# Optimization experiments

Measured on AMD Instinct MI355X. Metric: run time of the kernel, lower is better.

## Reference

```python
import jax, jax.numpy as jnp
import numpy as np

B, N, K = 8, 1024, 20


def _w(key, o, i):
    return jax.random.normal(key, (o, i), dtype=jnp.float32) * (1.0 / np.sqrt(i))


def setup_inputs() -> dict:
    key = jax.random.key(0)
    ks = iter(jax.random.split(key, 64))
    d = {"inputs": jax.random.normal(next(ks), (B, 3, N, 1), dtype=jnp.float32)}
    shapes = {
        "he_w1": (32, 12), "he_w2": (64, 32), "hn_w1": (32, 67), "hn_w2": (64, 32),
        "b1e_w1": (48, 192), "b1e_w2": (128, 48), "b1n_w1": (48, 192), "b1n_w2": (128, 48),
        "b2e_w1": (96, 384), "b2e_w2": (192, 96), "b2n_w1": (96, 320), "b2n_w2": (192, 96),
        "f_w": (512, 384), "p1_w": (256, 512), "p2_w": (128, 256), "p3_w": (40, 128),
    }
    for name, (o, i) in shapes.items():
        d[name] = _w(next(ks), o, i)
        d[name.replace("_w", "_b")] = jnp.zeros((o,), dtype=jnp.float32)
    return d


def _conv(x, w, b):
    # BasicConv with norm=None: 1x1 Conv2d + bias. x: [B,C,N,k]
    return jnp.einsum('bcnk,oc->bonk', x, w) + b[None, :, None, None]


def _conv_relu(x, w, b):
    return jax.nn.relu(_conv(x, w, b))


def _gather(x, idx):
    # batched_index_select: x [B,C,N,1], idx [B,N,k] -> [B,C,N,k]
    b, c, n, _ = x.shape
    k = idx.shape[-1]
    out = jnp.take_along_axis(x[:, :, :, 0], idx.reshape(b, 1, n * k), axis=2)
    return out.reshape(b, c, n, k)


def _knn(x, k):
    # DenseKnnGraph: x [B,C,N,1] -> (nn_idx, center_idx), each [B,N,k]
    xt = jnp.transpose(x[:, :, :, 0], (0, 2, 1))  # [B,N,C]
    sq = jnp.sum(xt * xt, axis=-1, keepdims=True)
    dist = sq - 2.0 * jnp.einsum('bnc,bmc->bnm', xt, xt) + jnp.transpose(sq, (0, 2, 1))
    _, nn_idx = jax.lax.top_k(-dist, k)
    center = jnp.broadcast_to(jnp.arange(x.shape[2])[None, :, None], nn_idx.shape)
    return nn_idx, center


def _mp(nf, e_ij, nn_idx, center, ew1, eb1, ew2, eb2, nw1, nb1, nw2, nb2):
    # MessagePassing block (Kearnes et al. style)
    h_i = _gather(nf, center)  # [B,Cin,N,k]
    h_j = _gather(nf, nn_idx)
    e_p = _conv_relu(_conv_relu(jnp.concatenate([e_ij, h_i, h_j], axis=1), ew1, eb1), ew2, eb2)
    m = jnp.broadcast_to(jnp.sum(e_p, axis=3, keepdims=True),
                         e_p.shape[:3] + (h_i.shape[-1],))
    h_p = _conv_relu(_conv_relu(jnp.concatenate([h_i, m], axis=1), nw1, nb1), nw2, nb2)
    return h_p[:, :, :, 0:1], e_p


def reference(inputs, he_w1, he_b1, he_w2, he_b2, hn_w1, hn_b1, hn_w2, hn_b2,
              b1e_w1, b1e_b1, b1e_w2, b1e_b2, b1n_w1, b1n_b1, b1n_w2, b1n_b2,
              b2e_w1, b2e_b1, b2e_w2, b2e_b2, b2n_w1, b2n_b1, b2n_w2, b2n_b2,
              f_w, f_b, p1_w, p1_b, p2_w, p2_b, p3_w, p3_b):
    nn_idx, center = _knn(inputs[:, 0:3], K)
    # initial edge features: (h_i, h_i - h_j) on xyz-KNN graph
    gh_i = _gather(inputs, center)
    gh_j = _gather(inputs, nn_idx)
    e_ij = jnp.concatenate([gh_i, gh_i - gh_j], axis=1)  # [B, 2*in, N, k]
    h1, e1 = _mp(inputs, e_ij, nn_idx, center, he_w1, he_b1, he_w2, he_b2, hn_w1, hn_b1, hn_w2, hn_b2)
    h2, e2 = _mp(h1, e1, nn_idx, center, b1e_w1, b1e_b1, b1e_w2, b1e_b2, b1n_w1, b1n_b1, b1n_w2, b1n_b2)
    h3, e3 = _mp(h2, e2, nn_idx, center, b2e_w1, b2e_b1, b2e_w2, b2e_b2, b2n_w1, b2n_b1, b2n_w2, b2n_b2)
    feats = jnp.concatenate([h1, h2, h3], axis=1)  # [B, 384, N, 1]
    fus = _conv_relu(feats, f_w, f_b)  # [B, 512, N, 1]
    pooled = jnp.max(fus, axis=(2, 3), keepdims=True)  # max_pool2d over [N,1]
    # prediction head (dropout = identity at inference)
    pred = _conv(_conv_relu(_conv_relu(pooled, p1_w, p1_b), p2_w, p2_b), p3_w, p3_b)
    return pred[:, :, :, 0], inputs  # (logits [B,n_classes,1], edge_features)
```

## Files before the change

kernel.cpp:

```cpp
#include <hip/hip_runtime.h>

#define BDIM 8
#define NDIM 1024
#define KNN 20

typedef unsigned short u16;
typedef float f32x4 __attribute__((ext_vector_type(4)));
typedef short short8 __attribute__((ext_vector_type(8)));
typedef unsigned short ushort8 __attribute__((ext_vector_type(8)));

__device__ inline u16 f2bf(float f) {
  unsigned u = __float_as_uint(f);
  unsigned r = (u + 0x7fffu + ((u >> 16) & 1u)) >> 16;
  return (u16)r;
}
__device__ inline float bf2f(u16 v) {
  return __uint_as_float(((unsigned)v) << 16);
}

__global__ __launch_bounds__(512) void knn_wcvt(
    const float* __restrict__ x, int* __restrict__ nn,
    const float* __restrict__ w1_3, const float* __restrict__ w2_3,
    const float* __restrict__ w1_2, const float* __restrict__ w2_2,
    const float* __restrict__ hn_w1, const float* __restrict__ f_w,
    const float* __restrict__ he_w1, const float* __restrict__ he_w2,
    const float* __restrict__ bn_w1, const float* __restrict__ bn_w2,
    const float* __restrict__ n2_w1, const float* __restrict__ n2_w2,
    u16* __restrict__ w1b3e, u16* __restrict__ wpq3, u16* __restrict__ w2b3,
    u16* __restrict__ w1b2e, u16* __restrict__ wpq2, u16* __restrict__ w2b2,
    float* __restrict__ w1p1, u16* __restrict__ fwb,
    u16* __restrict__ w1b1, u16* __restrict__ w2b1,
    u16* __restrict__ wn1b, u16* __restrict__ wn2b,
    u16* __restrict__ wn21b, u16* __restrict__ wn22b,
    int* __restrict__ pooled) {
  const int tid = threadIdx.x;
  if (blockIdx.x >= BDIM * 128) {
    const int idx = (blockIdx.x - BDIM * 128) * 512 + tid;
    if (idx < 512 * 384) fwb[idx] = f2bf(f_w[idx]);
    if (idx < 96 * 128) {
      int oc = idx >> 7, c = idx & 127;
      w1b3e[idx] = f2bf(w1_3[oc * 384 + c]);
    }
    if (idx < 192 * 128) {
      int n = idx >> 7, c = idx & 127;
      wpq3[idx] = f2bf(n < 96 ? w1_3[n * 384 + 128 + c]
                              : w1_3[(n - 96) * 384 + 256 + c]);
    }
    if (idx < 192 * 96) w2b3[idx] = f2bf(w2_3[idx]);
    if (idx < 48 * 64) {
      int oc = idx >> 6, c = idx & 63;
      w1b2e[idx] = f2bf(w1_2[oc * 192 + c]);
    }
    if (idx < 96 * 64) {
      int n = idx >> 6, c = idx & 63;
      wpq2[idx] = f2bf(n < 48 ? w1_2[n * 192 + 64 + c]
                              : w1_2[(n - 48) * 192 + 128 + c]);
    }
    if (idx < 128 * 64) {
      int oc = idx >> 6, i = idx & 63;
      w2b2[idx] = (i < 48) ? f2bf(w2_2[oc * 48 + i]) : (u16)0;
    }
    if (idx < 32 * 68) {
      int oc = idx / 68, c = idx - oc * 68;
      w1p1[idx] = (c < 67) ? hn_w1[oc * 67 + c] : 0.0f;
    }
    if (idx < 32 * 32) {
      int oc = idx >> 5, c = idx & 31;
      w1b1[idx] = (c < 12) ? f2bf(he_w1[oc * 12 + c]) : (u16)0;
    }
    if (idx < 64 * 32) w2b1[idx] = f2bf(he_w2[idx]);
    if (idx < 96 * 320) wn1b[idx] = f2bf(bn_w1[idx]);
    if (idx < 192 * 96) wn2b[idx] = f2bf(bn_w2[idx]);
    if (idx < 48 * 192) wn21b[idx] = f2bf(n2_w1[idx]);
    if (idx < 128 * 64) {
      int oc = idx >> 6, i = idx & 63;
      wn22b[idx] = (i < 48) ? f2bf(n2_w2[oc * 48 + i]) : (u16)0;
    }
    if (idx < BDIM * 512) pooled[idx] = 0;
    return;
  }
  {
#pragma clang fp contract(off)
    __shared__ float xs0[NDIM], xs1[NDIM], xs2[NDIM], sq[NDIM];
    const int lane = tid & 63;
    const int w = tid >> 6;
    const int b = blockIdx.x >> 7;
    const int n = ((blockIdx.x & 127) << 3) + w;
    for (int i = tid; i < NDIM; i += 512) {
      float a0 = x[(b * 3 + 0) * NDIM + i];
      float a1 = x[(b * 3 + 1) * NDIM + i];
      float a2 = x[(b * 3 + 2) * NDIM + i];
      xs0[i] = a0; xs1[i] = a1; xs2[i] = a2;
      sq[i] = (a0 * a0 + a1 * a1) + a2 * a2;
    }
    __syncthreads();
    const float xn0 = xs0[n], xn1 = xs1[n], xn2 = xs2[n], sqn = sq[n];
    float dl[16];
#pragma unroll
    for (int t = 0; t < 16; ++t) {
      int m = t * 64 + lane;
      float dot = (xn0 * xs0[m] + xn1 * xs1[m]) + xn2 * xs2[m];
      dl[t] = (sqn - 2.0f * dot) + sq[m];
    }
    int* nnrow = &nn[(b * NDIM + n) * KNN];
    for (int r = 0; r < KNN; ++r) {
      float bd = dl[0];
      int bt = 0;
#pragma unroll
      for (int t = 1; t < 16; ++t) {
        if (dl[t] < bd) { bd = dl[t]; bt = t; }
      }
      int bi = bt * 64 + lane;
#pragma unroll
      for (int off = 1; off < 64; off <<= 1) {
        float pd = __shfl_xor(bd, off);
        int pi = __shfl_xor(bi, off);
        if (pd < bd || (pd == bd && pi < bi)) { bd = pd; bi = pi; }
      }
      if (lane == 0) nnrow[r] = bi;
      if ((bi & 63) == lane) {
        int wt = bi >> 6;
#pragma unroll
        for (int t = 0; t < 16; ++t) {
          if (t == wt) dl[t] = 3.4e38f;
        }
      }
    }
  }
}

template <int PTS, int CE, int CMID, int COUT, bool WRITE_E, bool FIRST>
__global__ __launch_bounds__(256) void edge_mfma(
    const u16* __restrict__ eprev, const float* __restrict__ finput,
    const int* __restrict__ nnb, const u16* __restrict__ w1b,
    const float* __restrict__ b1v, const u16* __restrict__ w2b,
    const float* __restrict__ b2v, const u16* __restrict__ pq,
    u16* __restrict__ eout, float* __restrict__ mout) {
  constexpr int K2 = (CMID + 31) & ~31;
  constexpr int NPQ = 2 * CMID;
  constexpr int MT = PTS * KNN;
  constexpr int MTL = MT / 16;
  constexpr int XPB = CE + 8;
  constexpr int QYP = K2 + 8;
  __shared__ u16 Xs[MT * XPB];
  __shared__ u16 QY[MT * QYP];
  __shared__ float pld[FIRST ? 8 : PTS * CMID];
  const int tid = threadIdx.x;
  const int lane = tid & 63;
  const int wv = tid >> 6;
  const int q = lane >> 4;
  const int bn0 = blockIdx.x * PTS;
  const int b = bn0 >> 10;
  if constexpr (FIRST) {
    for (int idx = tid; idx < MT * (CE / 8); idx += 256) {
      int p = idx / (CE / 8), kc = idx - p * (CE / 8);
      int k0 = kc * 8;
      int bn = bn0 + p / KNN;
      int n = bn & (NDIM - 1);
      int j = nnb[(size_t)bn0 * KNN + p];
      ushort8 r;
#pragma unroll
      for (int t = 0; t < 8; ++t) {
        int c = k0 + t;
        float v = 0.0f;
        if (c < 3) v = finput[(b * 3 + c) * NDIM + n];
        else if (c < 6)
          v = finput[(b * 3 + c - 3) * NDIM + n] -
              finput[(b * 3 + c - 3) * NDIM + j];
        else if (c < 9) v = finput[(b * 3 + c - 6) * NDIM + n];
        else if (c < 12) v = finput[(b * 3 + c - 9) * NDIM + j];
        r[t] = f2bf(v);
      }
      *(ushort8*)&Xs[p * XPB + k0] = r;
    }
  } else {
    constexpr int KC = CE / 8;
    for (int ch = tid; ch < MT * KC; ch += 256) {
      int p = ch / KC, kc = ch - p * KC;
      int k0 = kc * 8;
      *(uint4*)&Xs[p * XPB + k0] =
          *(const uint4*)&eprev[((size_t)blockIdx.x * MT + p) * CE + k0];
    }
    constexpr int QC = CMID / 8;
    for (int i = tid; i < MT * QC; i += 256) {
      int p = i / QC, c8 = (i - p * QC) * 8;
      int j = nnb[(size_t)bn0 * KNN + p];
      *(uint4*)&QY[p * QYP + c8] =
          *(const uint4*)&pq[((size_t)(b << 10) + j) * NPQ + CMID + c8];
    }
    if constexpr (K2 != CMID) {
      constexpr int PC = (K2 - CMID) / 8;
      for (int i = tid; i < MT * PC; i += 256) {
        int p = i / PC, c8 = CMID + (i - p * PC) * 8;
        uint4 z = {0, 0, 0, 0};
        *(uint4*)&QY[p * QYP + c8] = z;
      }
    }
    for (int i = tid; i < PTS * CMID; i += 256) {
      int pt = i / CMID, c = i - pt * CMID;
      pld[i] = bf2f(pq[(size_t)(bn0 + pt) * NPQ + c]) + b1v[c];
    }
  }
  __syncthreads();
  {
    constexpr int NT1 = CMID / 16;
    constexpr int J1 = MTL * NT1;
    constexpr int KS1 = CE / 32;
    for (int job = wv; job < J1; job += 4) {
      int mt = job / NT1, nt = job - mt * NT1;
      int row = mt * 16 + (lane & 15);
      int ncol = nt * 16 + (lane & 15);
      int kb = q * 8;
      f32x4 acc = {0.f, 0.f, 0.f, 0.f};
      const u16* ap = &Xs[row * XPB + kb];
      const u16* bp = &w1b[(size_t)ncol * CE + kb];
#pragma unroll
      for (int ks = 0; ks < KS1; ++ks) {
        short8 a = *(const short8*)(ap + ks * 32);
        short8 bb = *(const short8*)(bp + ks * 32);
        acc = __builtin_amdgcn_mfma_f32_16x16x32_bf16(a, bb, acc, 0, 0, 0);
      }
      int m0 = mt * 16 + q * 4;
      if constexpr (FIRST) {
        float bias = b1v[ncol];
#pragma unroll
        for (int r = 0; r < 4; ++r) {
          float yv = fmaxf(acc[r] + bias, 0.0f);
          QY[(m0 + r) * QYP + ncol] = f2bf(yv);
        }
      } else {
        int pt = m0 / KNN;
        float padd = pld[pt * CMID + ncol];
#pragma unroll
        for (int r = 0; r < 4; ++r) {
          int m = m0 + r;
          float qadd = bf2f(QY[m * QYP + ncol]);
          float yv = fmaxf(acc[r] + padd + qadd, 0.0f);
          QY[m * QYP + ncol] = f2bf(yv);
        }
      }
    }
  }
  __syncthreads();
  {
    constexpr int NT2 = COUT / 16;
    constexpr int KS2 = K2 / 32;
    for (int nt = wv; nt < NT2; nt += 4) {
      int ncol = nt * 16 + (lane & 15);
      int kb = q * 8;
      short8 bfrag[KS2];
      const u16* bp = &w2b[(size_t)ncol * K2 + kb];
#pragma unroll
      for (int ks = 0; ks < KS2; ++ks)
        bfrag[ks] = *(const short8*)(bp + ks * 32);
      float bias = b2v[ncol];
      float s[PTS];
#pragma unroll
      for (int pt = 0; pt < PTS; ++pt) s[pt] = 0.0f;
#pragma unroll
      for (int mt = 0; mt < MTL; ++mt) {
        f32x4 acc = {0.f, 0.f, 0.f, 0.f};
        const u16* ap = &QY[(mt * 16 + (lane & 15)) * QYP + kb];
#pragma unroll
        for (int ks = 0; ks < KS2; ++ks) {
          short8 a = *(const short8*)(ap + ks * 32);
          acc = __builtin_amdgcn_mfma_f32_16x16x32_bf16(a, bfrag[ks], acc, 0, 0, 0);
        }
        int m0 = mt * 16 + q * 4;
        float part = 0.0f;
#pragma unroll
        for (int r = 0; r < 4; ++r) {
          float yv = fmaxf(acc[r] + bias, 0.0f);
          if (WRITE_E)
            eout[((size_t)blockIdx.x * MT + m0 + r) * COUT + ncol] = f2bf(yv);
          part += yv;
        }
        int ptA = (4 * mt) / 5;
        int ptB = (4 * mt + 3) / 5;
        int qb = 5 * ptB - 4 * mt;
#pragma unroll
        for (int pt2 = 0; pt2 < PTS; ++pt2) {
          if (pt2 == ptA && ptA == ptB) s[pt2] += part;
          else if (pt2 == ptA) s[pt2] += (q < qb) ? part : 0.0f;
          else if (pt2 == ptB) s[pt2] += (q < qb) ? 0.0f : part;
        }
      }
#pragma unroll
      for (int pt = 0; pt < PTS; ++pt) {
        float sv = s[pt];
        sv += __shfl_xor(sv, 16);
        sv += __shfl_xor(sv, 32);
        if (lane < 16)
          mout[(size_t)(bn0 + pt) * COUT + nt * 16 + lane] = sv;
      }
    }
  }
}

template <int TP, int CH, int CM, int CINP, int CMID, int COUT, int NPQ, bool FIRSTH>
__global__ __launch_bounds__(256) void node_conv(
    const float* __restrict__ h, const float* __restrict__ inputs,
    const float* __restrict__ mbuf, const float* __restrict__ w1p,
    const float* __restrict__ b1v, const float* __restrict__ w2,
    const float* __restrict__ b2v, float* __restrict__ hout,
    const u16* __restrict__ wpq, u16* __restrict__ pq) {
  constexpr int CIN = CH + CM;
  constexpr int XP = CINP + 4;
  constexpr int Y1P = CMID + 4;
  constexpr int PG = TP / 4;
  constexpr int HP = COUT + 8;
  __shared__ float Xs[TP * XP];
  __shared__ float Y1s[TP * Y1P];
  __shared__ u16 Hb[(NPQ > 0) ? TP * HP : 8];
  const int tid = threadIdx.x;
  const int bn0 = blockIdx.x * TP;
  if constexpr (FIRSTH) {
    for (int idx = tid; idx < TP * CIN; idx += 256) {
      int p = idx / CIN, c = idx - p * CIN;
      int bn = bn0 + p;
      int b = bn >> 10, n = bn & (NDIM - 1);
      Xs[p * XP + c] = (c < CH) ? inputs[(b * 3 + c) * NDIM + n]
                                : mbuf[(size_t)bn * CM + (c - CH)];
    }
    if constexpr (CINP > CIN) {
      constexpr int PAD = CINP - CIN;
      for (int idx = tid; idx < TP * PAD; idx += 256) {
        int p = idx / PAD, c = CIN + idx % PAD;
        Xs[p * XP + c] = 0.0f;
      }
    }
  } else {
    constexpr int C4 = CIN / 4;
    for (int idx = tid; idx < TP * C4; idx += 256) {
      int p = idx / C4, c = (idx - p * C4) * 4;
      int bn = bn0 + p;
      float4 v = (c < CH) ? *(const float4*)&h[(size_t)bn * CH + c]
                          : *(const float4*)&mbuf[(size_t)bn * CM + (c - CH)];
      *(float4*)&Xs[p * XP + c] = v;
    }
  }
  __syncthreads();
  {
    constexpr int NT1 = PG * (CMID / 4);
    for (int t = tid; t < NT1; t += 256) {
      int pg = t % PG, og = t / PG;
      float acc[4][4];
#pragma unroll
      for (int j = 0; j < 4; ++j) {
        float bj = b1v[og * 4 + j];
#pragma unroll
        for (int i = 0; i < 4; ++i) acc[i][j] = bj;
      }
      for (int cin = 0; cin < CINP; cin += 4) {
        float4 xr[4], wr[4];
#pragma unroll
        for (int i = 0; i < 4; ++i)
          xr[i] = *(const float4*)&Xs[(pg * 4 + i) * XP + cin];
#pragma unroll
        for (int j = 0; j < 4; ++j)
          wr[j] = *(const float4*)&w1p[(size_t)(og * 4 + j) * CINP + cin];
#pragma unroll
        for (int i = 0; i < 4; ++i)
#pragma unroll
          for (int j = 0; j < 4; ++j) {
            acc[i][j] += xr[i].x * wr[j].x;
            acc[i][j] += xr[i].y * wr[j].y;
            acc[i][j] += xr[i].z * wr[j].z;
            acc[i][j] += xr[i].w * wr[j].w;
          }
      }
#pragma unroll
      for (int i = 0; i < 4; ++i)
#pragma unroll
        for (int j = 0; j < 4; ++j)
          Y1s[(pg * 4 + i) * Y1P + og * 4 + j] = fmaxf(acc[i][j], 0.0f);
    }
  }
  __syncthreads();
  {
    constexpr int NT2 = PG * (COUT / 4);
    for (int t = tid; t < NT2; t += 256) {
      int pg = t % PG, og = t / PG;
      float acc[4][4];
#pragma unroll
      for (int j = 0; j < 4; ++j) {
        float bj = b2v[og * 4 + j];
#pragma unroll
        for (int i = 0; i < 4; ++i) acc[i][j] = bj;
      }
      for (int cin = 0; cin < CMID; cin += 4) {
        float4 xr[4], wr[4];
#pragma unroll
        for (int i = 0; i < 4; ++i)
          xr[i] = *(const float4*)&Y1s[(pg * 4 + i) * Y1P + cin];
#pragma unroll
        for (int j = 0; j < 4; ++j)
          wr[j] = *(const float4*)&w2[(size_t)(og * 4 + j) * CMID + cin];
#pragma unroll
        for (int i = 0; i < 4; ++i)
#pragma unroll
          for (int j = 0; j < 4; ++j) {
            acc[i][j] += xr[i].x * wr[j].x;
            acc[i][j] += xr[i].y * wr[j].y;
            acc[i][j] += xr[i].z * wr[j].z;
            acc[i][j] += xr[i].w * wr[j].w;
          }
      }
#pragma unroll
      for (int i = 0; i < 4; ++i) {
        int bn = bn0 + pg * 4 + i;
#pragma unroll
        for (int j = 0; j < 4; ++j) {
          float v = fmaxf(acc[i][j], 0.0f);
          hout[(size_t)bn * COUT + og * 4 + j] = v;
          if constexpr (NPQ > 0) Hb[(pg * 4 + i) * HP + og * 4 + j] = f2bf(v);
        }
      }
    }
  }
  if constexpr (NPQ > 0) {
    __syncthreads();
    const int lane = tid & 63;
    const int wv = tid >> 6;
    constexpr int NT = NPQ / 16;
    constexpr int JOBS = (TP / 16) * NT;
    constexpr int KS = COUT / 32;
    for (int job = wv; job < JOBS; job += 4) {
      int mt = job / NT, nt = job - mt * NT;
      int row = mt * 16 + (lane & 15);
      int ncol = nt * 16 + (lane & 15);
      int kb = (lane >> 4) * 8;
      f32x4 acc = {0.f, 0.f, 0.f, 0.f};
      const u16* ap = &Hb[row * HP + kb];
      const u16* bp = &wpq[(size_t)ncol * COUT + kb];
#pragma unroll
      for (int ks = 0; ks < KS; ++ks) {
        short8 a = *(const short8*)(ap + ks * 32);
        short8 bb = *(const short8*)(bp + ks * 32);
        acc = __builtin_amdgcn_mfma_f32_16x16x32_bf16(a, bb, acc, 0, 0, 0);
      }
      int m0 = mt * 16 + (lane >> 4) * 4;
#pragma unroll
      for (int r = 0; r < 4; ++r)
        pq[(size_t)(bn0 + m0 + r) * NPQ + ncol] = f2bf(acc[r]);
    }
  }
}

__global__ __launch_bounds__(256) void node2_mfma(
    const float* __restrict__ h1, const float* __restrict__ m2,
    const u16* __restrict__ w1b, const float* __restrict__ b1v,
    const u16* __restrict__ w2b, const float* __restrict__ b2v,
    float* __restrict__ h2out, const u16* __restrict__ wpq,
    u16* __restrict__ pq) {
  constexpr int TP = 32, XP = 200, Y1P = 72, HP = 136;
  __shared__ u16 Xb[TP * XP];
  __shared__ u16 Y1[TP * Y1P];
  __shared__ u16 Hb[TP * HP];
  const int tid = threadIdx.x;
  const int lane = tid & 63;
  const int wv = tid >> 6;
  const int q = lane >> 4;
  const int bn0 = blockIdx.x * TP;
  for (int i = tid; i < TP * 24; i += 256) {
    int p = i / 24, kc = i - p * 24;
    int k0 = kc * 8;
    const float* src = (k0 < 64) ? &h1[(size_t)(bn0 + p) * 64 + k0]
                                 : &m2[(size_t)(bn0 + p) * 128 + (k0 - 64)];
    float4 f0 = *(const float4*)src;
    float4 f1 = *(const float4*)(src + 4);
    ushort8 r;
    r[0] = f2bf(f0.x); r[1] = f2bf(f0.y); r[2] = f2bf(f0.z); r[3] = f2bf(f0.w);
    r[4] = f2bf(f1.x); r[5] = f2bf(f1.y); r[6] = f2bf(f1.z); r[7] = f2bf(f1.w);
    *(ushort8*)&Xb[p * XP + k0] = r;
  }
  for (int i = tid; i < TP * 2; i += 256) {
    int p = i >> 1, c8 = 48 + (i & 1) * 8;
    ushort8 z = {0, 0, 0, 0, 0, 0, 0, 0};
    *(ushort8*)&Y1[p * Y1P + c8] = z;
  }
  __syncthreads();
  for (int job = wv; job < 6; job += 4) {
    int mt = job / 3, nt = job - mt * 3;
    int row = mt * 16 + (lane & 15);
    int ncol = nt * 16 + (lane & 15);
    int kb = q * 8;
    f32x4 acc = {0.f, 0.f, 0.f, 0.f};
    const u16* ap = &Xb[row * XP + kb];
    const u16* bp = &w1b[(size_t)ncol * 192 + kb];
#pragma unroll
    for (int ks = 0; ks < 6; ++ks) {
      short8 a = *(const short8*)(ap + ks * 32);
      short8 bb = *(const short8*)(bp + ks * 32);
      acc = __builtin_amdgcn_mfma_f32_16x16x32_bf16(a, bb, acc, 0, 0, 0);
    }
    float bias = b1v[ncol];
    int m0 = mt * 16 + q * 4;
#pragma unroll
    for (int r = 0; r < 4; ++r)
      Y1[(m0 + r) * Y1P + ncol] = f2bf(fmaxf(acc[r] + bias, 0.0f));
  }
  __syncthreads();
  for (int job = wv; job < 16; job += 4) {
    int mt = job / 8, nt = job - mt * 8;
    int row = mt * 16 + (lane & 15);
    int ncol = nt * 16 + (lane & 15);
    int kb = q * 8;
    f32x4 acc = {0.f, 0.f, 0.f, 0.f};
    const u16* ap = &Y1[row * Y1P + kb];
    const u16* bp = &w2b[(size_t)ncol * 64 + kb];
#pragma unroll
    for (int ks = 0; ks < 2; ++ks) {
      short8 a = *(const short8*)(ap + ks * 32);
      short8 bb = *(const short8*)(bp + ks * 32);
      acc = __builtin_amdgcn_mfma_f32_16x16x32_bf16(a, bb, acc, 0, 0, 0);
    }
    float bias = b2v[ncol];
    int m0 = mt * 16 + q * 4;
#pragma unroll
    for (int r = 0; r < 4; ++r) {
      float v = fmaxf(acc[r] + bias, 0.0f);
      h2out[(size_t)(bn0 + m0 + r) * 128 + ncol] = v;
      Hb[(m0 + r) * HP + ncol] = f2bf(v);
    }
  }
  __syncthreads();
  for (int job = wv; job < 24; job += 4) {
    int mt = job / 12, nt = job - mt * 12;
    int row = mt * 16 + (lane & 15);
    int ncol = nt * 16 + (lane & 15);
    int kb = q * 8;
    f32x4 acc = {0.f, 0.f, 0.f, 0.f};
    const u16* ap = &Hb[row * HP + kb];
    const u16* bp = &wpq[(size_t)ncol * 128 + kb];
#pragma unroll
    for (int ks = 0; ks < 4; ++ks) {
      short8 a = *(const short8*)(ap + ks * 32);
      short8 bb = *(const short8*)(bp + ks * 32);
      acc = __builtin_amdgcn_mfma_f32_16x16x32_bf16(a, bb, acc, 0, 0, 0);
    }
    int m0 = mt * 16 + q * 4;
#pragma unroll
    for (int r = 0; r < 4; ++r)
      pq[(size_t)(bn0 + m0 + r) * 192 + ncol] = f2bf(acc[r]);
  }
}

__global__ __launch_bounds__(256) void fuse_pool_mfma(
    const float* __restrict__ h1, const float* __restrict__ h2,
    const float* __restrict__ m3, const u16* __restrict__ wn1b,
    const float* __restrict__ bn1v, const u16* __restrict__ wn2b,
    const float* __restrict__ bn2v, const u16* __restrict__ fwb,
    const float* __restrict__ fb, int* __restrict__ pooled) {
  constexpr int TP = 32;
  constexpr int XNP = 328;
  constexpr int Y1NP = 104;
  constexpr int XPB = 392;
  __shared__ __align__(16) char smem[TP * XPB * 2];
  u16* Xs = (u16*)smem;
  u16* Xn = (u16*)smem;
  __shared__ u16 Y1n[TP * Y1NP];
  __shared__ int pmax[512];
  const int tid = threadIdx.x;
  const int lane = tid & 63;
  const int wv = tid >> 6;
  const int q = lane >> 4;
  const int bn0 = blockIdx.x * TP;
  const int b = bn0 >> 10;
  for (int i = tid; i < 512; i += 256) pmax[i] = 0;
  for (int i = tid; i < TP * 41; i += 256) {
    int p = i / 41, kc = i - p * 41;
    int k0 = kc * 8;
    ushort8 r;
    if (kc < 16) {
      const float* src = &h2[(size_t)(bn0 + p) * 128 + k0];
      float4 f0 = *(const float4*)src;
      float4 f1 = *(const float4*)(src + 4);
      r[0] = f2bf(f0.x); r[1] = f2bf(f0.y); r[2] = f2bf(f0.z); r[3] = f2bf(f0.w);
      r[4] = f2bf(f1.x); r[5] = f2bf(f1.y); r[6] = f2bf(f1.z); r[7] = f2bf(f1.w);
    } else if (kc < 40) {
      const float* src = &m3[(size_t)(bn0 + p) * 192 + (k0 - 128)];
      float4 f0 = *(const float4*)src;
      float4 f1 = *(const float4*)(src + 4);
      r[0] = f2bf(f0.x); r[1] = f2bf(f0.y); r[2] = f2bf(f0.z); r[3] = f2bf(f0.w);
      r[4] = f2bf(f1.x); r[5] = f2bf(f1.y); r[6] = f2bf(f1.z); r[7] = f2bf(f1.w);
    } else {
#pragma unroll
      for (int t = 0; t < 8; ++t) r[t] = 0;
    }
    *(ushort8*)&Xn[p * XNP + k0] = r;
  }
  __syncthreads();
  for (int job = wv; job < 12; job += 4) {
    int mt = job / 6, nt = job - mt * 6;
    int row = mt * 16 + (lane & 15);
    int ncol = nt * 16 + (lane & 15);
    int kb = q * 8;
    f32x4 acc = {0.f, 0.f, 0.f, 0.f};
    const u16* ap = &Xn[row * XNP + kb];
    const u16* bp = &wn1b[(size_t)ncol * 320 + kb];
#pragma unroll
    for (int ks = 0; ks < 10; ++ks) {
      short8 a = *(const short8*)(ap + ks * 32);
      short8 bb = *(const short8*)(bp + ks * 32);
      acc = __builtin_amdgcn_mfma_f32_16x16x32_bf16(a, bb, acc, 0, 0, 0);
    }
    float bias = bn1v[ncol];
    int m0 = mt * 16 + q * 4;
#pragma unroll
    for (int r = 0; r < 4; ++r)
      Y1n[(m0 + r) * Y1NP + ncol] = f2bf(fmaxf(acc[r] + bias, 0.0f));
  }
  __syncthreads();
  for (int i = tid; i < TP * 24; i += 256) {
    int p = i / 24, kc = i - p * 24;
    int k0 = kc * 8;
    const float* src = (k0 < 64) ? &h1[(size_t)(bn0 + p) * 64 + k0]
                                 : &h2[(size_t)(bn0 + p) * 128 + (k0 - 64)];
    float4 f0 = *(const float4*)src;
    float4 f1 = *(const float4*)(src + 4);
    ushort8 r;
    r[0] = f2bf(f0.x); r[1] = f2bf(f0.y); r[2] = f2bf(f0.z); r[3] = f2bf(f0.w);
    r[4] = f2bf(f1.x); r[5] = f2bf(f1.y); r[6] = f2bf(f1.z); r[7] = f2bf(f1.w);
    *(ushort8*)&Xs[p * XPB + k0] = r;
  }
  if (tid < TP) {
    ushort8 z = {0, 0, 0, 0, 0, 0, 0, 0};
    *(ushort8*)&Xs[tid * XPB + 384] = z;
  }
  for (int job = wv; job < 24; job += 4) {
    int mt = job / 12, nt = job - mt * 12;
    int row = mt * 16 + (lane & 15);
    int ncol = nt * 16 + (lane & 15);
    int kb = q * 8;
    f32x4 acc = {0.f, 0.f, 0.f, 0.f};
    const u16* ap = &Y1n[row * Y1NP + kb];
    const u16* bp = &wn2b[(size_t)ncol * 96 + kb];
#pragma unroll
    for (int ks = 0; ks < 3; ++ks) {
      short8 a = *(const short8*)(ap + ks * 32);
      short8 bb = *(const short8*)(bp + ks * 32);
      acc = __builtin_amdgcn_mfma_f32_16x16x32_bf16(a, bb, acc, 0, 0, 0);
    }
    float bias = bn2v[ncol];
    int m0 = mt * 16 + q * 4;
#pragma unroll
    for (int r = 0; r < 4; ++r)
      Xs[(m0 + r) * XPB + 192 + ncol] = f2bf(fmaxf(acc[r] + bias, 0.0f));
  }
  __syncthreads();
  for (int job = wv; job < 64; job += 4) {
    int mt = job / 32, nt = job - mt * 32;
    int row = mt * 16 + (lane & 15);
    int ncol = nt * 16 + (lane & 15);
    int kb = q * 8;
    f32x4 acc = {0.f, 0.f, 0.f, 0.f};
    const u16* ap = &Xs[row * XPB + kb];
    const u16* bp = &fwb[(size_t)ncol * 384 + kb];
#pragma unroll
    for (int ks = 0; ks < 12; ++ks) {
      short8 a = *(const short8*)(ap + ks * 32);
      short8 bb = *(const short8*)(bp + ks * 32);
      acc = __builtin_amdgcn_mfma_f32_16x16x32_bf16(a, bb, acc, 0, 0, 0);
    }
    float bias = fb[ncol];
    float v = fmaxf(fmaxf(acc[0], acc[1]), fmaxf(acc[2], acc[3]));
    v = fmaxf(v + bias, 0.0f);
    v = fmaxf(v, __shfl_xor(v, 16));
    v = fmaxf(v, __shfl_xor(v, 32));
    if (lane < 16) atomicMax(&pmax[ncol], __float_as_int(v));
  }
  __syncthreads();
  for (int i = tid; i < 512; i += 256)
    atomicMax(&pooled[b * 512 + i], pmax[i]);
}

__global__ __launch_bounds__(256) void head_kernel(
    const int* __restrict__ pooledi, const float* __restrict__ p1w,
    const float* __restrict__ p1b, const float* __restrict__ p2w,
    const float* __restrict__ p2b, const float* __restrict__ p3w,
    const float* __restrict__ p3b, const float* __restrict__ inputs,
    float* __restrict__ out) {
  const int tid = threadIdx.x;
  if (blockIdx.x >= BDIM) {
    int idx = (blockIdx.x - BDIM) * 256 + tid;
    if (idx < (BDIM * 3 * NDIM) / 4) {
      const float4* src = (const float4*)inputs;
      float4* dst = (float4*)(out + BDIM * 40);
      dst[idx] = src[idx];
    }
    return;
  }
  __shared__ float xs[512], y1[256], y2[128];
  const int b = blockIdx.x;
  for (int i = tid; i < 512; i += 256) xs[i] = __int_as_float(pooledi[b * 512 + i]);
  __syncthreads();
  {
    float acc = p1b[tid];
    for (int c = 0; c < 512; ++c) acc += xs[c] * p1w[tid * 512 + c];
    y1[tid] = fmaxf(acc, 0.0f);
  }
  __syncthreads();
  if (tid < 128) {
    float acc = p2b[tid];
    for (int c = 0; c < 256; ++c) acc += y1[c] * p2w[tid * 256 + c];
    y2[tid] = fmaxf(acc, 0.0f);
  }
  __syncthreads();
  if (tid < 40) {
    float acc = p3b[tid];
    for (int c = 0; c < 128; ++c) acc += y2[c] * p3w[tid * 128 + c];
    out[b * 40 + tid] = acc;
  }
}

extern "C" void kernel_launch(void* const* d_in, const int* in_sizes, int n_in,
                              void* d_out, int out_size, void* d_ws,
                              size_t ws_size, hipStream_t stream) {
  const float* inputs = (const float*)d_in[0];
  const float* he_w1 = (const float*)d_in[1];
  const float* he_b1 = (const float*)d_in[2];
  const float* he_w2 = (const float*)d_in[3];
  const float* he_b2 = (const float*)d_in[4];
  const float* hn_w1 = (const float*)d_in[5];
  const float* hn_b1 = (const float*)d_in[6];
  const float* hn_w2 = (const float*)d_in[7];
  const float* hn_b2 = (const float*)d_in[8];
  const float* b1e_w1 = (const float*)d_in[9];
  const float* b1e_b1 = (const float*)d_in[10];
  const float* b1e_w2 = (const float*)d_in[11];
  const float* b1e_b2 = (const float*)d_in[12];
  const float* b1n_w1 = (const float*)d_in[13];
  const float* b1n_b1 = (const float*)d_in[14];
  const float* b1n_w2 = (const float*)d_in[15];
  const float* b1n_b2 = (const float*)d_in[16];
  const float* b2e_w1 = (const float*)d_in[17];
  const float* b2e_b1 = (const float*)d_in[18];
  const float* b2e_w2 = (const float*)d_in[19];
  const float* b2e_b2 = (const float*)d_in[20];
  const float* b2n_w1 = (const float*)d_in[21];
  const float* b2n_b1 = (const float*)d_in[22];
  const float* b2n_w2 = (const float*)d_in[23];
  const float* b2n_b2 = (const float*)d_in[24];
  const float* f_w = (const float*)d_in[25];
  const float* f_b = (const float*)d_in[26];
  const float* p1_w = (const float*)d_in[27];
  const float* p1_b = (const float*)d_in[28];
  const float* p2_w = (const float*)d_in[29];
  const float* p2_b = (const float*)d_in[30];
  const float* p3_w = (const float*)d_in[31];
  const float* p3_b = (const float*)d_in[32];
  float* out = (float*)d_out;

  char* ws = (char*)d_ws;
  size_t off = 0;
  auto alloc = [&](size_t bytes) {
    void* p = ws + off;
    off += (bytes + 255) & ~(size_t)255;
    return p;
  };
  int* nn = (int*)alloc((size_t)BDIM * NDIM * KNN * 4);
  float* m1 = (float*)alloc((size_t)BDIM * NDIM * 64 * 4);
  float* h1 = (float*)alloc((size_t)BDIM * NDIM * 64 * 4);
  u16* e1 = (u16*)alloc((size_t)BDIM * NDIM * KNN * 64 * 2);
  float* m2 = (float*)alloc((size_t)BDIM * NDIM * 128 * 4);
  float* h2 = (float*)alloc((size_t)BDIM * NDIM * 128 * 4);
  u16* e2 = (u16*)alloc((size_t)BDIM * NDIM * KNN * 128 * 2);
  float* m3 = (float*)alloc((size_t)BDIM * NDIM * 192 * 4);
  u16* pq2 = (u16*)alloc((size_t)BDIM * NDIM * 96 * 2);
  u16* pq3 = (u16*)alloc((size_t)BDIM * NDIM * 192 * 2);
  int* pooled = (int*)alloc((size_t)BDIM * 512 * 4);
  u16* w1b3e = (u16*)alloc((size_t)96 * 128 * 2);
  u16* wpq3 = (u16*)alloc((size_t)192 * 128 * 2);
  u16* w2b3 = (u16*)alloc((size_t)192 * 96 * 2);
  u16* w1b2e = (u16*)alloc((size_t)48 * 64 * 2);
  u16* wpq2 = (u16*)alloc((size_t)96 * 64 * 2);
  u16* w2b2 = (u16*)alloc((size_t)128 * 64 * 2);
  float* w1p1 = (float*)alloc((size_t)32 * 68 * 4);
  u16* fwb = (u16*)alloc((size_t)512 * 384 * 2);
  u16* w1b1 = (u16*)alloc((size_t)32 * 32 * 2);
  u16* w2b1 = (u16*)alloc((size_t)64 * 32 * 2);
  u16* wn1b = (u16*)alloc((size_t)96 * 320 * 2);
  u16* wn2b = (u16*)alloc((size_t)192 * 96 * 2);
  u16* wn21b = (u16*)alloc((size_t)48 * 192 * 2);
  u16* wn22b = (u16*)alloc((size_t)128 * 64 * 2);

  knn_wcvt<<<BDIM * 128 + 384, 512, 0, stream>>>(
      inputs, nn, b2e_w1, b2e_w2, b1e_w1, b1e_w2, hn_w1, f_w, he_w1, he_w2,
      b2n_w1, b2n_w2, b1n_w1, b1n_w2, w1b3e, wpq3, w2b3, w1b2e, wpq2, w2b2,
      w1p1, fwb, w1b1, w2b1, wn1b, wn2b, wn21b, wn22b, pooled);

  edge_mfma<4, 32, 32, 64, true, true><<<BDIM * NDIM / 4, 256, 0, stream>>>(
      nullptr, inputs, nn, w1b1, he_b1, w2b1, he_b2, nullptr, e1, m1);
  node_conv<64, 3, 64, 68, 32, 64, 96, true><<<BDIM * NDIM / 64, 256, 0, stream>>>(
      nullptr, inputs, m1, w1p1, hn_b1, hn_w2, hn_b2, h1, wpq2, pq2);

  edge_mfma<4, 64, 48, 128, true, false><<<BDIM * NDIM / 4, 256, 0, stream>>>(
      e1, nullptr, nn, w1b2e, b1e_b1, w2b2, b1e_b2, pq2, e2, m2);
  node2_mfma<<<BDIM * NDIM / 32, 256, 0, stream>>>(
      h1, m2, wn21b, b1n_b1, wn22b, b1n_b2, h2, wpq3, pq3);

  edge_mfma<4, 128, 96, 192, false, false><<<BDIM * NDIM / 4, 256, 0, stream>>>(
      e2, nullptr, nn, w1b3e, b2e_b1, w2b3, b2e_b2, pq3, nullptr, m3);

  fuse_pool_mfma<<<BDIM * NDIM / 32, 256, 0, stream>>>(
      h1, h2, m3, wn1b, b2n_b1, wn2b, b2n_b2, fwb, f_b, pooled);
  head_kernel<<<BDIM + 24, 256, 0, stream>>>(pooled, p1_w, p1_b, p2_w, p2_b,
                                             p3_w, p3_b, inputs, out);
}
```

Before: 214.5 us.

## Fuse first edge MLP into the KNN kernel using in-LDS neighbor indices

The first message-passing edge MLP (12->32->64 with ReLU and the neighbor sum into m1) now runs inside the KNN blocks, right after each block picks its 8 points' neighbors. It reads coordinates and indices straight from shared memory, which removes a separate kernel launch and the global reloads of nn and inputs. The first-layer edge weights are converted to bf16 inside each block instead of being staged in global memory. In exchange the KNN kernel uses more LDS and registers, which may lower its occupancy.

```diff
diff --git a/kernel.cpp b/kernel.cpp
--- a/kernel.cpp
+++ b/kernel.cpp
@@ -24,14 +24,15 @@
     const float* __restrict__ w1_2, const float* __restrict__ w2_2,
     const float* __restrict__ hn_w1, const float* __restrict__ f_w,
     const float* __restrict__ he_w1, const float* __restrict__ he_w2,
+    const float* __restrict__ he_b1, const float* __restrict__ he_b2,
     const float* __restrict__ bn_w1, const float* __restrict__ bn_w2,
     const float* __restrict__ n2_w1, const float* __restrict__ n2_w2,
     u16* __restrict__ w1b3e, u16* __restrict__ wpq3, u16* __restrict__ w2b3,
     u16* __restrict__ w1b2e, u16* __restrict__ wpq2, u16* __restrict__ w2b2,
     float* __restrict__ w1p1, u16* __restrict__ fwb,
-    u16* __restrict__ w1b1, u16* __restrict__ w2b1,
     u16* __restrict__ wn1b, u16* __restrict__ wn2b,
     u16* __restrict__ wn21b, u16* __restrict__ wn22b,
+    u16* __restrict__ e1out, float* __restrict__ m1out,
     int* __restrict__ pooled) {
   const int tid = threadIdx.x;
   if (blockIdx.x >= BDIM * 128) {
@@ -64,11 +65,6 @@
       int oc = idx / 68, c = idx - oc * 68;
       w1p1[idx] = (c < 67) ? hn_w1[oc * 67 + c] : 0.0f;
     }
-    if (idx < 32 * 32) {
-      int oc = idx >> 5, c = idx & 31;
-      w1b1[idx] = (c < 12) ? f2bf(he_w1[oc * 12 + c]) : (u16)0;
-    }
-    if (idx < 64 * 32) w2b1[idx] = f2bf(he_w2[idx]);
     if (idx < 96 * 320) wn1b[idx] = f2bf(bn_w1[idx]);
     if (idx < 192 * 96) wn2b[idx] = f2bf(bn_w2[idx]);
     if (idx < 48 * 192) wn21b[idx] = f2bf(n2_w1[idx]);
@@ -82,10 +78,15 @@
   {
 #pragma clang fp contract(off)
     __shared__ float xs0[NDIM], xs1[NDIM], xs2[NDIM], sq[NDIM];
+    __shared__ int nns_l[8 * KNN];
+    __shared__ u16 Xe[160 * 40];
+    __shared__ u16 QYe[160 * 40];
     const int lane = tid & 63;
     const int w = tid >> 6;
+    const int q = lane >> 4;
     const int b = blockIdx.x >> 7;
-    const int n = ((blockIdx.x & 127) << 3) + w;
+    const int nbase = (blockIdx.x & 127) << 3;
+    const int n = nbase + w;
     for (int i = tid; i < NDIM; i += 512) {
       float a0 = x[(b * 3 + 0) * NDIM + i];
       float a1 = x[(b * 3 + 1) * NDIM + i];
@@ -117,7 +118,10 @@
         int pi = __shfl_xor(bi, off);
         if (pd < bd || (pd == bd && pi < bi)) { bd = pd; bi = pi; }
       }
-      if (lane == 0) nnrow[r] = bi;
+      if (lane == 0) {
+        nnrow[r] = bi;
+        nns_l[w * KNN + r] = bi;
+      }
       if ((bi & 63) == lane) {
         int wt = bi >> 6;
 #pragma unroll
@@ -126,16 +130,122 @@
         }
       }
     }
+    __syncthreads();
+    const size_t bn0g = (size_t)b * NDIM + nbase;
+    for (int idx = tid; idx < 160 * 4; idx += 512) {
+      int p = idx >> 2, kc = idx & 3;
+      int k0 = kc * 8;
+      ushort8 r;
+      if (kc < 2) {
+        int lp = p / KNN;
+        int pn = nbase + lp;
+        int j = nns_l[p];
+#pragma unroll
+        for (int t = 0; t < 8; ++t) {
+          int c = k0 + t;
+          float v = 0.0f;
+          if (c < 3) v = (c == 0 ? xs0[pn] : (c == 1 ? xs1[pn] : xs2[pn]));
+          else if (c < 6) {
+            int cc = c - 3;
+            float ai = (cc == 0 ? xs0[pn] : (cc == 1 ? xs1[pn] : xs2[pn]));
+            float aj = (cc == 0 ? xs0[j] : (cc == 1 ? xs1[j] : xs2[j]));
+            v = ai - aj;
+          } else if (c < 9) {
+            int cc = c - 6;
+            v = (cc == 0 ? xs0[pn] : (cc == 1 ? xs1[pn] : xs2[pn]));
+          } else if (c < 12) {
+            int cc = c - 9;
+            v = (cc == 0 ? xs0[j] : (cc == 1 ? xs1[j] : xs2[j]));
+          }
+          r[t] = f2bf(v);
+        }
+      } else {
+#pragma unroll
+        for (int t = 0; t < 8; ++t) r[t] = 0;
+      }
+      *(ushort8*)&Xe[p * 40 + k0] = r;
+    }
+    __syncthreads();
+    for (int job = w; job < 20; job += 8) {
+      int mt = job >> 1, nt = job & 1;
+      int row = mt * 16 + (lane & 15);
+      int ncol = nt * 16 + (lane & 15);
+      int kb = q * 8;
+      ushort8 bfr;
+#pragma unroll
+      for (int t = 0; t < 8; ++t) {
+        int c = kb + t;
+        bfr[t] = (c < 12) ? f2bf(he_w1[ncol * 12 + c]) : (u16)0;
+      }
+      short8 a = *(const short8*)&Xe[row * 40 + kb];
+      short8 bb = *(short8*)&bfr;
+      f32x4 acc = {0.f, 0.f, 0.f, 0.f};
+      acc = __builtin_amdgcn_mfma_f32_16x16x32_bf16(a, bb, acc, 0, 0, 0);
+      float bias = he_b1[ncol];
+      int m0 = mt * 16 + q * 4;
+#pragma unroll
+      for (int r = 0; r < 4; ++r)
+        QYe[(m0 + r) * 40 + ncol] = f2bf(fmaxf(acc[r] + bias, 0.0f));
+    }
+    __syncthreads();
+    {
+      int nt = w & 3, half = w >> 2;
+      int ncol = nt * 16 + (lane & 15);
+      int kb = q * 8;
+      ushort8 bfr;
+      {
+        const float* s = &he_w2[ncol * 32 + kb];
+        float4 f0 = *(const float4*)s;
+        float4 f1 = *(const float4*)(s + 4);
+        bfr[0] = f2bf(f0.x); bfr[1] = f2bf(f0.y); bfr[2] = f2bf(f0.z); bfr[3] = f2bf(f0.w);
+        bfr[4] = f2bf(f1.x); bfr[5] = f2bf(f1.y); bfr[6] = f2bf(f1.z); bfr[7] = f2bf(f1.w);
+      }
+      short8 bb = *(short8*)&bfr;
+      float bias = he_b2[ncol];
+      float s[4] = {0.f, 0.f, 0.f, 0.f};
+#pragma unroll
+      for (int mi = 0; mi < 5; ++mi) {
+        int mt = half * 5 + mi;
+        short8 a = *(const short8*)&QYe[(mt * 16 + (lane & 15)) * 40 + kb];
+        f32x4 acc = {0.f, 0.f, 0.f, 0.f};
+        acc = __builtin_amdgcn_mfma_f32_16x16x32_bf16(a, bb, acc, 0, 0, 0);
+        int m0 = mt * 16 + q * 4;
+        float part = 0.0f;
+#pragma unroll
+        for (int r = 0; r < 4; ++r) {
+          float yv = fmaxf(acc[r] + bias, 0.0f);
+          e1out[(bn0g * KNN + m0 + r) * 64 + ncol] = f2bf(yv);
+          part += yv;
+        }
+        int ptA = (4 * mt) / 5 - half * 4;
+        int ptB = (4 * mt + 3) / 5 - half * 4;
+        int qb = 5 * ((4 * mt + 3) / 5) - 4 * mt;
+#pragma unroll
+        for (int p2 = 0; p2 < 4; ++p2) {
+          if (p2 == ptA && ptA == ptB) s[p2] += part;
+          else if (p2 == ptA) s[p2] += (q < qb) ? part : 0.0f;
+          else if (p2 == ptB) s[p2] += (q < qb) ? 0.0f : part;
+        }
+      }
+#pragma unroll
+      for (int p2 = 0; p2 < 4; ++p2) {
+        float sv = s[p2];
+        sv += __shfl_xor(sv, 16);
+        sv += __shfl_xor(sv, 32);
+        if (lane < 16)
+          m1out[(bn0g + half * 4 + p2) * 64 + nt * 16 + lane] = sv;
+      }
+    }
   }
 }
 
-template <int PTS, int CE, int CMID, int COUT, bool WRITE_E, bool FIRST>
+template <int PTS, int CE, int CMID, int COUT, bool WRITE_E>
 __global__ __launch_bounds__(256) void edge_mfma(
-    const u16* __restrict__ eprev, const float* __restrict__ finput,
-    const int* __restrict__ nnb, const u16* __restrict__ w1b,
-    const float* __restrict__ b1v, const u16* __restrict__ w2b,
-    const float* __restrict__ b2v, const u16* __restrict__ pq,
-    u16* __restrict__ eout, float* __restrict__ mout) {
+    const u16* __restrict__ eprev, const int* __restrict__ nnb,
+    const u16* __restrict__ w1b, const float* __restrict__ b1v,
+    const u16* __restrict__ w2b, const float* __restrict__ b2v,
+    const u16* __restrict__ pq, u16* __restrict__ eout,
+    float* __restrict__ mout) {
   constexpr int K2 = (CMID + 31) & ~31;
   constexpr int NPQ = 2 * CMID;
   constexpr int MT = PTS * KNN;
@@ -144,36 +254,14 @@
   constexpr int QYP = K2 + 8;
   __shared__ u16 Xs[MT * XPB];
   __shared__ u16 QY[MT * QYP];
-  __shared__ float pld[FIRST ? 8 : PTS * CMID];
+  __shared__ float pld[PTS * CMID];
   const int tid = threadIdx.x;
   const int lane = tid & 63;
   const int wv = tid >> 6;
   const int q = lane >> 4;
   const int bn0 = blockIdx.x * PTS;
   const int b = bn0 >> 10;
-  if constexpr (FIRST) {
-    for (int idx = tid; idx < MT * (CE / 8); idx += 256) {
-      int p = idx / (CE / 8), kc = idx - p * (CE / 8);
-      int k0 = kc * 8;
-      int bn = bn0 + p / KNN;
-      int n = bn & (NDIM - 1);
-      int j = nnb[(size_t)bn0 * KNN + p];
-      ushort8 r;
-#pragma unroll
-      for (int t = 0; t < 8; ++t) {
-        int c = k0 + t;
-        float v = 0.0f;
-        if (c < 3) v = finput[(b * 3 + c) * NDIM + n];
-        else if (c < 6)
-          v = finput[(b * 3 + c - 3) * NDIM + n] -
-              finput[(b * 3 + c - 3) * NDIM + j];
-        else if (c < 9) v = finput[(b * 3 + c - 6) * NDIM + n];
-        else if (c < 12) v = finput[(b * 3 + c - 9) * NDIM + j];
-        r[t] = f2bf(v);
-      }
-      *(ushort8*)&Xs[p * XPB + k0] = r;
-    }
-  } else {
+  {
     constexpr int KC = CE / 8;
     for (int ch = tid; ch < MT * KC; ch += 256) {
       int p = ch / KC, kc = ch - p * KC;
@@ -221,23 +309,14 @@
         acc = __builtin_amdgcn_mfma_f32_16x16x32_bf16(a, bb, acc, 0, 0, 0);
       }
       int m0 = mt * 16 + q * 4;
-      if constexpr (FIRST) {
-        float bias = b1v[ncol];
-#pragma unroll
-        for (int r = 0; r < 4; ++r) {
-          float yv = fmaxf(acc[r] + bias, 0.0f);
-          QY[(m0 + r) * QYP + ncol] = f2bf(yv);
-        }
-      } else {
-        int pt = m0 / KNN;
-        float padd = pld[pt * CMID + ncol];
-#pragma unroll
-        for (int r = 0; r < 4; ++r) {
-          int m = m0 + r;
-          float qadd = bf2f(QY[m * QYP + ncol]);
-          float yv = fmaxf(acc[r] + padd + qadd, 0.0f);
-          QY[m * QYP + ncol] = f2bf(yv);
-        }
+      int pt = m0 / KNN;
+      float padd = pld[pt * CMID + ncol];
+#pragma unroll
+      for (int r = 0; r < 4; ++r) {
+        int m = m0 + r;
+        float qadd = bf2f(QY[m * QYP + ncol]);
+        float yv = fmaxf(acc[r] + padd + qadd, 0.0f);
+        QY[m * QYP + ncol] = f2bf(yv);
       }
     }
   }
@@ -778,8 +857,6 @@
   u16* w2b2 = (u16*)alloc((size_t)128 * 64 * 2);
   float* w1p1 = (float*)alloc((size_t)32 * 68 * 4);
   u16* fwb = (u16*)alloc((size_t)512 * 384 * 2);
-  u16* w1b1 = (u16*)alloc((size_t)32 * 32 * 2);
-  u16* w2b1 = (u16*)alloc((size_t)64 * 32 * 2);
   u16* wn1b = (u16*)alloc((size_t)96 * 320 * 2);
   u16* wn2b = (u16*)alloc((size_t)192 * 96 * 2);
   u16* wn21b = (u16*)alloc((size_t)48 * 192 * 2);
@@ -787,21 +864,19 @@
 
   knn_wcvt<<<BDIM * 128 + 384, 512, 0, stream>>>(
       inputs, nn, b2e_w1, b2e_w2, b1e_w1, b1e_w2, hn_w1, f_w, he_w1, he_w2,
-      b2n_w1, b2n_w2, b1n_w1, b1n_w2, w1b3e, wpq3, w2b3, w1b2e, wpq2, w2b2,
-      w1p1, fwb, w1b1, w2b1, wn1b, wn2b, wn21b, wn22b, pooled);
-
-  edge_mfma<4, 32, 32, 64, true, true><<<BDIM * NDIM / 4, 256, 0, stream>>>(
-      nullptr, inputs, nn, w1b1, he_b1, w2b1, he_b2, nullptr, e1, m1);
+      he_b1, he_b2, b2n_w1, b2n_w2, b1n_w1, b1n_w2, w1b3e, wpq3, w2b3, w1b2e,
+      wpq2, w2b2, w1p1, fwb, wn1b, wn2b, wn21b, wn22b, e1, m1, pooled);
+
   node_conv<64, 3, 64, 68, 32, 64, 96, true><<<BDIM * NDIM / 64, 256, 0, stream>>>(
       nullptr, inputs, m1, w1p1, hn_b1, hn_w2, hn_b2, h1, wpq2, pq2);
 
-  edge_mfma<4, 64, 48, 128, true, false><<<BDIM * NDIM / 4, 256, 0, stream>>>(
-      e1, nullptr, nn, w1b2e, b1e_b1, w2b2, b1e_b2, pq2, e2, m2);
+  edge_mfma<4, 64, 48, 128, true><<<BDIM * NDIM / 4, 256, 0, stream>>>(
+      e1, nn, w1b2e, b1e_b1, w2b2, b1e_b2, pq2, e2, m2);
   node2_mfma<<<BDIM * NDIM / 32, 256, 0, stream>>>(
       h1, m2, wn21b, b1n_b1, wn22b, b1n_b2, h2, wpq3, pq3);
 
-  edge_mfma<4, 128, 96, 192, false, false><<<BDIM * NDIM / 4, 256, 0, stream>>>(
-      e2, nullptr, nn, w1b3e, b2e_b1, w2b3, b2e_b2, pq3, nullptr, m3);
+  edge_mfma<4, 128, 96, 192, false><<<BDIM * NDIM / 4, 256, 0, stream>>>(
+      e2, nn, w1b3e, b2e_b1, w2b3, b2e_b2, pq3, nullptr, m3);
 
   fuse_pool_mfma<<<BDIM * NDIM / 32, 256, 0, stream>>>(
       h1, h2, m3, wn1b, b2n_b1, wn2b, b2n_b2, fwb, f_b, pooled);
```

Result: slower. 221.9 us (+3.5%).
